# Optimization experiments

Measured on AMD Instinct MI355X. Metric: run time of the kernel, lower is better.

The kernel has to match this reference:

```python
import jax, jax.numpy as jnp
import numpy as np

N_NODES = 50000
N_EDGES = 800000
N_GRAPHS = 512
D = 128
NUM_GIN_LAYERS = 4
BN_EPS = 1e-5


def setup_inputs() -> dict:
    key = jax.random.key(0)
    ks = jax.random.split(key, 10)
    h = jax.random.normal(ks[0], (N_NODES, D), dtype=jnp.float32)
    src = jax.random.randint(ks[1], (N_EDGES,), 0, N_NODES, dtype=jnp.int32)
    dst = jax.random.randint(ks[2], (N_EDGES,), 0, N_NODES, dtype=jnp.int32)
    graph_id = jnp.sort(jax.random.randint(ks[3], (N_NODES,), 0, N_GRAPHS, dtype=jnp.int32))
    scale = 1.0 / np.sqrt(D)
    W1s = jax.random.normal(ks[4], (NUM_GIN_LAYERS, D, D), dtype=jnp.float32) * scale
    W2s = jax.random.normal(ks[5], (NUM_GIN_LAYERS, D, D), dtype=jnp.float32) * scale
    bn1_g = jnp.ones((NUM_GIN_LAYERS, D), jnp.float32)
    bn1_b = jnp.zeros((NUM_GIN_LAYERS, D), jnp.float32)
    bn2_g = jnp.ones((NUM_GIN_LAYERS, D), jnp.float32)
    bn2_b = jnp.zeros((NUM_GIN_LAYERS, D), jnp.float32)
    pred_W = jax.random.normal(ks[6], (NUM_GIN_LAYERS + 1, D, D), dtype=jnp.float32) * scale
    pred_b = jnp.zeros((NUM_GIN_LAYERS + 1, D), jnp.float32)
    return {"h": h, "src": src, "dst": dst, "graph_id": graph_id,
            "W1s": W1s, "W2s": W2s, "bn1_g": bn1_g, "bn1_b": bn1_b,
            "bn2_g": bn2_g, "bn2_b": bn2_b, "pred_W": pred_W, "pred_b": pred_b}


def _batch_norm(x, gamma, beta):
    # training-mode BN over the node axis
    mean = jnp.mean(x, axis=0)
    var = jnp.var(x, axis=0)
    return (x - mean) * jax.lax.rsqrt(var + BN_EPS) * gamma + beta


def reference(h, src, dst, graph_id, W1s, W2s, bn1_g, bn1_b, bn2_g, bn2_b, pred_W, pred_b):
    n = h.shape[0]
    hidden_rep = [h]
    for i in range(NUM_GIN_LAYERS):
        # GINConv, eps=0: (1+eps)*h + sum over in-neighbors (scatter-sum over edges)
        agg = jax.ops.segment_sum(h[src], dst, num_segments=n)
        z = h + agg
        # two-layer MLP: Linear(no bias) -> BN -> ReLU -> Linear(no bias)
        z = jax.nn.relu(_batch_norm(z @ W1s[i], bn1_g[i], bn1_b[i]))
        z = z @ W2s[i]
        # outer BN + ReLU
        h = jax.nn.relu(_batch_norm(z, bn2_g[i], bn2_b[i]))
        hidden_rep.append(h)
    # graph readout: per-graph max pool over each layer's representation,
    # then per-layer linear prediction summed (dropout is identity in eval)
    score = jnp.zeros((N_GRAPHS, pred_W.shape[-1]), h.dtype)
    for i, hr in enumerate(hidden_rep):
        pooled = jax.ops.segment_max(hr, graph_id, num_segments=N_GRAPHS,
                                     indices_are_sorted=True)
        score = score + pooled @ pred_W[i] + pred_b[i]
    return score
```

## Files before the change

kernel.cpp:

```cpp
#include <hip/hip_runtime.h>

#define N_NODES 50000
#define N_EDGES 800000
#define N_GRAPHS 512
#define DIM 128
#define NLAYERS 4
#define BN_EPS 1e-5f
#define NTILE (N_NODES / 16)
#define POIS ((int)0xAAAAAAAA)
#define NREP 8

#define NBUCK 80
#define CAPB 12288
#define EPB 1600
#define NBIN 500

typedef unsigned short u16;
typedef float f32x2 __attribute__((ext_vector_type(2)));
typedef float f32x4 __attribute__((ext_vector_type(4)));
typedef short bf16x8 __attribute__((ext_vector_type(8)));

__device__ __forceinline__ short f2bs(float f) {
    union { float f; unsigned u; } v; v.f = f;
    unsigned r = v.u + 0x7FFFu + ((v.u >> 16) & 1u);
    return (short)(r >> 16);
}
__device__ __forceinline__ float bu2f(unsigned u) {
    union { unsigned u; float f; } v; v.u = u << 16;
    return v.f;
}
__device__ __forceinline__ unsigned packbf(float x, float y) {
    return ((unsigned)(u16)f2bs(y) << 16) | (unsigned)(u16)f2bs(x);
}

__device__ __forceinline__ void foldbn(const float* __restrict__ st,
                                       const float* __restrict__ gamma,
                                       const float* __restrict__ beta,
                                       float* absm, int tid) {
    if (tid < 128) {
        float s = 0.f, sq = 0.f;
#pragma unroll
        for (int j = 0; j < NREP; j++) {
            s += st[j * 256 + tid];
            sq += st[j * 256 + 128 + tid];
        }
        float mean = s * (1.f / N_NODES);
        float var = sq * (1.f / N_NODES) - mean * mean;
        float a = gamma[tid] * rsqrtf(var + BN_EPS);
        absm[tid] = a;
        absm[DIM + tid] = beta[tid] - mean * a;
    }
}

__global__ __launch_bounds__(256) void k_prepbin(const float* __restrict__ h,
                                                 const float* __restrict__ W1s,
                                                 const float* __restrict__ W2s,
                                                 const int* __restrict__ gid,
                                                 const int* __restrict__ src,
                                                 const int* __restrict__ dst,
                                                 unsigned* __restrict__ hb,
                                                 short* __restrict__ wt,
                                                 int* __restrict__ gs, int* __restrict__ ge,
                                                 unsigned* __restrict__ eb,
                                                 int* __restrict__ gcur) {
    __shared__ int hist[NBUCK], base[NBUCK], lcur[NBUCK];
    int bid = blockIdx.x, tid = threadIdx.x;
    if (bid >= 6250) {
        int bbid = bid - 6250;
        if (tid < NBUCK) hist[tid] = 0;
        __syncthreads();
        int e0 = bbid * EPB;
        unsigned rec[7]; int rb[7];
#pragma unroll
        for (int k = 0; k < 7; k++) {
            int idx = tid + k * 256;
            rb[k] = -1;
            if (idx < EPB) {
                int s = src[e0 + idx], d = dst[e0 + idx];
                rec[k] = ((unsigned)d << 16) | (unsigned)s;
                int x = d / 6250;
                int sub = (d - x * 6250) / 625;
                rb[k] = x + 8 * sub;
                atomicAdd(&hist[rb[k]], 1);
            }
        }
        __syncthreads();
        if (tid < NBUCK) {
            int old = atomicAdd(&gcur[tid], hist[tid]);
            base[tid] = old - POIS;
            lcur[tid] = 0;
        }
        __syncthreads();
#pragma unroll
        for (int k = 0; k < 7; k++) {
            if (rb[k] >= 0) {
                int p = atomicAdd(&lcur[rb[k]], 1);
                eb[rb[k] * CAPB + base[rb[k]] + p] = rec[k];
            }
        }
        return;
    }
    int gtid = bid * 256 + tid;
    {
        f32x4 v = *(const f32x4*)(h + gtid * 4);
        uint2 pp;
        pp.x = packbf(v.x, v.y);
        pp.y = packbf(v.z, v.w);
        *(uint2*)(hb + gtid * 2) = pp;
    }
    if (gtid < 8 * 16384) {
        int m = gtid >> 14, r = gtid & 16383, n = r >> 7, k = r & 127;
        const float* W = (m < 4) ? (W1s + m * 16384) : (W2s + (m - 4) * 16384);
        wt[gtid] = f2bs(W[k * DIM + n]);
    }
    if (gtid < N_NODES) {
        int g = gid[gtid];
        if (gtid == 0 || gid[gtid - 1] != g) gs[g] = gtid;
        if (gtid == N_NODES - 1 || gid[gtid + 1] != g) ge[g] = gtid + 1;
    }
}

__global__ __launch_bounds__(256) void k_fillpool0(const unsigned* __restrict__ eb,
                                                   const int* __restrict__ gcur,
                                                   int* __restrict__ begA,
                                                   int* __restrict__ endA,
                                                   u16* __restrict__ eix,
                                                   const unsigned* __restrict__ hb,
                                                   const int* __restrict__ gs,
                                                   const int* __restrict__ ge,
                                                   float* __restrict__ pool4) {
    __shared__ int hist[625], begL[625], sm[256];
    __shared__ f32x2 psm[256];
    int bid = blockIdx.x, tid = threadIdx.x;
    if (bid < NBUCK) {
        int x = bid & 7, sub = bid >> 3;
        int n0 = x * 6250 + sub * 625;
        int mybase = 0, mycnt = 0;
        for (int r = 0; r < NBUCK; r++) {
            int c = gcur[r] - POIS;
            int rx = r & 7, rs = r >> 3;
            if (rx < x || (rx == x && rs < sub)) mybase += c;
            if (r == bid) mycnt = c;
        }
        for (int i = tid; i < 625; i += 256) hist[i] = 0;
        __syncthreads();
        const unsigned* my = eb + bid * CAPB;
        for (int i = tid; i < mycnt; i += 256) {
            int dl = (int)(my[i] >> 16) - n0;
            atomicAdd(&hist[dl], 1);
        }
        __syncthreads();
        int carry = 0;
        for (int c = 0; c < 3; c++) {
            int idx = c * 256 + tid;
            int v = (idx < 625) ? hist[idx] : 0;
            int xv = v;
            sm[tid] = xv; __syncthreads();
#pragma unroll
            for (int d = 1; d < 256; d <<= 1) {
                int y = (tid >= d) ? sm[tid - d] : 0;
                __syncthreads();
                sm[tid] = xv = xv + y;
                __syncthreads();
            }
            if (idx < 625) begL[idx] = mybase + carry + xv - v;
            int ct = sm[255];
            __syncthreads();
            carry += ct;
        }
        __syncthreads();
        for (int i = tid; i < 625; i += 256) {
            int b = begL[i];
            begA[n0 + i] = b;
            endA[n0 + i] = b + hist[i];
        }
        __syncthreads();
        for (int i = tid; i < mycnt; i += 256) {
            unsigned rc = my[i];
            int dl = (int)(rc >> 16) - n0;
            int p = atomicAdd(&begL[dl], 1);
            eix[p] = (u16)(rc & 0xFFFFu);
        }
        return;
    }
    int pb = bid - NBUCK;
    int g = pb >> 2, sub = pb & 3;
    int ci = tid & 63, ro = tid >> 6;
    int beg = gs[g], end = ge[g];
    f32x2 mx = (f32x2){-3.402823e38f, -3.402823e38f};
    if (beg >= 0 && end <= N_NODES) {
        for (int r = beg + sub * 4 + ro; r < end; r += 16) {
            unsigned w = hb[r * 64 + ci];
            mx.x = fmaxf(mx.x, bu2f(w & 0xffffu));
            mx.y = fmaxf(mx.y, bu2f(w >> 16));
        }
    }
    psm[tid] = mx;
    __syncthreads();
    if (ro == 0) {
        f32x2 mA0 = psm[tid], mA1 = psm[tid + 64];
        f32x2 mB0 = psm[tid + 128], mB1 = psm[tid + 192];
        f32x2 a, b;
        a.x = fmaxf(mA0.x, mA1.x); a.y = fmaxf(mA0.y, mA1.y);
        b.x = fmaxf(mB0.x, mB1.x); b.y = fmaxf(mB0.y, mB1.y);
        *(f32x2*)(pool4 + (pb * 2) * DIM + ci * 2) = a;
        *(f32x2*)(pool4 + (pb * 2 + 1) * DIM + ci * 2) = b;
    }
}

__global__ __launch_bounds__(128) void k_gather0(const unsigned* __restrict__ hp,
                                                 const int* __restrict__ begA,
                                                 const int* __restrict__ endA,
                                                 const u16* __restrict__ eix,
                                                 unsigned* __restrict__ Za) {
    int node = blockIdx.x * 2 + (threadIdx.x >> 6);
    int lane = threadIdx.x & 63;
    float ax = 0.f, ay = 0.f;
#define TX(w, rx, ry)                                         \
    {                                                         \
        rx += bu2f((w) & 0xffffu); ry += bu2f((w) >> 16);     \
    }
    TX(hp[node * 64 + lane], ax, ay);
    int beg = begA[node];
    int end = endA[node];
    int e = beg;
    if ((e & 1) && e < end) {
        unsigned ww = hp[eix[e] * 64 + lane];
        TX(ww, ax, ay);
        e++;
    }
    const unsigned* ep = (const unsigned*)eix;
    for (; e + 8 <= end; e += 8) {
        int k = e >> 1;
        unsigned p0 = ep[k], p1 = ep[k + 1], p2 = ep[k + 2], p3 = ep[k + 3];
        unsigned w0 = hp[(p0 & 0xffffu) * 64 + lane], w1 = hp[(p0 >> 16) * 64 + lane];
        unsigned w2 = hp[(p1 & 0xffffu) * 64 + lane], w3 = hp[(p1 >> 16) * 64 + lane];
        unsigned w4 = hp[(p2 & 0xffffu) * 64 + lane], w5 = hp[(p2 >> 16) * 64 + lane];
        unsigned w6 = hp[(p3 & 0xffffu) * 64 + lane], w7 = hp[(p3 >> 16) * 64 + lane];
        TX(w0, ax, ay); TX(w1, ax, ay); TX(w2, ax, ay); TX(w3, ax, ay);
        TX(w4, ax, ay); TX(w5, ax, ay); TX(w6, ax, ay); TX(w7, ax, ay);
    }
    for (; e + 2 <= end; e += 2) {
        unsigned pp = ep[e >> 1];
        unsigned w0 = hp[(pp & 0xffffu) * 64 + lane], w1 = hp[(pp >> 16) * 64 + lane];
        TX(w0, ax, ay); TX(w1, ax, ay);
    }
    if (e < end) {
        unsigned ww = hp[eix[e] * 64 + lane];
        TX(ww, ax, ay);
    }
#undef TX
    Za[node * 64 + lane] = packbf(ax, ay);
}

__global__ __launch_bounds__(128) void k_poolgather(const unsigned* __restrict__ Zr,
                                                    const float* __restrict__ stats,
                                                    const float* __restrict__ gamma,
                                                    const float* __restrict__ beta,
                                                    const int* __restrict__ gs,
                                                    const int* __restrict__ ge,
                                                    float* __restrict__ pool4,
                                                    const int* __restrict__ begA,
                                                    const int* __restrict__ endA,
                                                    const u16* __restrict__ eix,
                                                    unsigned* __restrict__ Za) {
    __shared__ float absm[256];
    __shared__ f32x2 psm[128];
    int bid = blockIdx.x, tid = threadIdx.x;
    foldbn(stats, gamma, beta, absm, tid);
    __syncthreads();
    if (bid < 4096) {
        int g = bid >> 3, sub = bid & 7;
        int ci = tid & 63, ro = tid >> 6;
        int beg = gs[g], end = ge[g];
        f32x2 a = *(const f32x2*)(absm + ci * 2);
        f32x2 b = *(const f32x2*)(absm + DIM + ci * 2);
        f32x2 mx = (f32x2){-3.402823e38f, -3.402823e38f};
        if (beg >= 0 && end <= N_NODES) {
            for (int r = beg + sub * 2 + ro; r < end; r += 16) {
                unsigned w = Zr[r * 64 + ci];
                float vx = fmaxf(a.x * bu2f(w & 0xffffu) + b.x, 0.f);
                float vy = fmaxf(a.y * bu2f(w >> 16) + b.y, 0.f);
                mx.x = fmaxf(mx.x, vx);
                mx.y = fmaxf(mx.y, vy);
            }
        }
        psm[tid] = mx;
        __syncthreads();
        if (ro == 0) {
            f32x2 m0 = psm[tid], m1 = psm[tid + 64];
            m0.x = fmaxf(m0.x, m1.x);
            m0.y = fmaxf(m0.y, m1.y);
            *(f32x2*)(pool4 + bid * DIM + ci * 2) = m0;
        }
        return;
    }
    int node = (bid - 4096) * 2 + (tid >> 6);
    int lane = tid & 63;
    float a0 = absm[2 * lane], a1 = absm[2 * lane + 1];
    float b0 = absm[DIM + 2 * lane], b1 = absm[DIM + 2 * lane + 1];
#define TX(w, rx, ry)                                         \
    {                                                         \
        float _x = bu2f((w) & 0xffffu), _y = bu2f((w) >> 16); \
        _x = fmaxf(a0 * _x + b0, 0.f);                        \
        _y = fmaxf(a1 * _y + b1, 0.f);                        \
        rx += _x; ry += _y;                                   \
    }
    float ax = 0.f, ay = 0.f;
    TX(Zr[node * 64 + lane], ax, ay);
    int beg = begA[node];
    int end = endA[node];
    int e = beg;
    if ((e & 1) && e < end) {
        unsigned ww = Zr[eix[e] * 64 + lane];
        TX(ww, ax, ay);
        e++;
    }
    const unsigned* ep = (const unsigned*)eix;
    for (; e + 8 <= end; e += 8) {
        int k = e >> 1;
        unsigned p0 = ep[k], p1 = ep[k + 1], p2 = ep[k + 2], p3 = ep[k + 3];
        unsigned w0 = Zr[(p0 & 0xffffu) * 64 + lane], w1 = Zr[(p0 >> 16) * 64 + lane];
        unsigned w2 = Zr[(p1 & 0xffffu) * 64 + lane], w3 = Zr[(p1 >> 16) * 64 + lane];
        unsigned w4 = Zr[(p2 & 0xffffu) * 64 + lane], w5 = Zr[(p2 >> 16) * 64 + lane];
        unsigned w6 = Zr[(p3 & 0xffffu) * 64 + lane], w7 = Zr[(p3 >> 16) * 64 + lane];
        TX(w0, ax, ay); TX(w1, ax, ay); TX(w2, ax, ay); TX(w3, ax, ay);
        TX(w4, ax, ay); TX(w5, ax, ay); TX(w6, ax, ay); TX(w7, ax, ay);
    }
    for (; e + 2 <= end; e += 2) {
        unsigned pp = ep[e >> 1];
        unsigned w0 = Zr[(pp & 0xffffu) * 64 + lane], w1 = Zr[(pp >> 16) * 64 + lane];
        TX(w0, ax, ay); TX(w1, ax, ay);
    }
    if (e < end) {
        unsigned ww = Zr[eix[e] * 64 + lane];
        TX(ww, ax, ay);
    }
#undef TX
    Za[node * 64 + lane] = packbf(ax, ay);
}

template <bool XF>
__global__ __launch_bounds__(256, 3) void k_gemm(const unsigned* __restrict__ X,
                                                 const short* __restrict__ wt,
                                                 const float* __restrict__ statsPrev,
                                                 const float* __restrict__ gamma,
                                                 const float* __restrict__ beta,
                                                 unsigned* __restrict__ OUT,
                                                 float* __restrict__ statsDst) {
    __shared__ short wls[128][136];
    __shared__ float tbuf[4][16][68];
    __shared__ float absm[256];
    __shared__ float smst[256];
    const int tid = threadIdx.x, bid = blockIdx.x;
    const int lane = tid & 63, wid = tid >> 6;
    const int ln15 = lane & 15, q = lane >> 4;
    float (*buf)[68] = tbuf[wid];

    int tile = bid * 4 + wid;
    uint4 xv[4];
    if (tile < NTILE) {
        const unsigned* xr = X + (tile * 16 + ln15) * 64;
#pragma unroll
        for (int s = 0; s < 4; s++) xv[s] = *(const uint4*)(xr + s * 16 + q * 4);
    }
    {
        int r = tid >> 1, hh = tid & 1;
        const uint4* s4 = (const uint4*)(wt + r * 128 + hh * 64);
        uint4* d4 = (uint4*)&wls[r][hh * 64];
#pragma unroll
        for (int i = 0; i < 8; i++) d4[i] = s4[i];
    }
    if (XF) foldbn(statsPrev, gamma, beta, absm, tid);
    smst[tid] = 0.f;
    __syncthreads();

    float sac[8], qac[8];
#pragma unroll
    for (int t = 0; t < 8; t++) { sac[t] = 0.f; qac[t] = 0.f; }

    if (tile < NTILE) {
        bf16x8 afr[4];
        if constexpr (!XF) {
#pragma unroll
            for (int s = 0; s < 4; s++) afr[s] = *(bf16x8*)&xv[s];
        } else {
            f32x4 aA[4], aB[4], bA[4], bB[4];
#pragma unroll
            for (int s = 0; s < 4; s++) {
                int k0 = s * 32 + q * 8;
                aA[s] = *(const f32x4*)(absm + k0);
                aB[s] = *(const f32x4*)(absm + k0 + 4);
                bA[s] = *(const f32x4*)(absm + DIM + k0);
                bB[s] = *(const f32x4*)(absm + DIM + k0 + 4);
            }
#pragma unroll
            for (int s = 0; s < 4; s++) {
                uint4 w4v = xv[s];
                float v0 = fmaxf(aA[s].x * bu2f(w4v.x & 0xffffu) + bA[s].x, 0.f);
                float v1 = fmaxf(aA[s].y * bu2f(w4v.x >> 16) + bA[s].y, 0.f);
                float v2 = fmaxf(aA[s].z * bu2f(w4v.y & 0xffffu) + bA[s].z, 0.f);
                float v3 = fmaxf(aA[s].w * bu2f(w4v.y >> 16) + bA[s].w, 0.f);
                float v4 = fmaxf(aB[s].x * bu2f(w4v.z & 0xffffu) + bB[s].x, 0.f);
                float v5 = fmaxf(aB[s].y * bu2f(w4v.z >> 16) + bB[s].y, 0.f);
                float v6 = fmaxf(aB[s].z * bu2f(w4v.w & 0xffffu) + bB[s].z, 0.f);
                float v7 = fmaxf(aB[s].w * bu2f(w4v.w >> 16) + bB[s].w, 0.f);
                bf16x8 a;
                a[0] = f2bs(v0); a[1] = f2bs(v1); a[2] = f2bs(v2); a[3] = f2bs(v3);
                a[4] = f2bs(v4); a[5] = f2bs(v5); a[6] = f2bs(v6); a[7] = f2bs(v7);
                afr[s] = a;
            }
        }
        f32x4 acc[8];
#pragma unroll
        for (int t = 0; t < 8; t++) acc[t] = (f32x4){0.f, 0.f, 0.f, 0.f};
#pragma unroll
        for (int s = 0; s < 4; s++) {
#pragma unroll
            for (int t = 0; t < 8; t++) {
                bf16x8 bfr = *(const bf16x8*)&wls[t * 16 + ln15][s * 32 + q * 8];
                acc[t] = __builtin_amdgcn_mfma_f32_16x16x32_bf16(afr[s], bfr, acc[t], 0, 0, 0);
            }
        }
#pragma unroll
        for (int t = 0; t < 8; t++) {
            float s_l = 0.f, q_l = 0.f;
#pragma unroll
            for (int r = 0; r < 4; r++) {
                float v = acc[t][r];
                s_l += v;
                q_l += v * v;
            }
            s_l += __shfl_xor(s_l, 16); s_l += __shfl_xor(s_l, 32);
            q_l += __shfl_xor(q_l, 16); q_l += __shfl_xor(q_l, 32);
            sac[t] = s_l;
            qac[t] = q_l;
        }
#pragma unroll
        for (int ch = 0; ch < 2; ch++) {
#pragma unroll
            for (int t2 = 0; t2 < 4; t2++) {
                int t = ch * 4 + t2;
#pragma unroll
                for (int r = 0; r < 4; r++)
                    buf[q * 4 + r][t2 * 16 + ln15] = acc[t][r];
            }
#pragma unroll
            for (int rr = 0; rr < 4; rr++) {
                int lr = rr * 4 + q;
                f32x4 v = *(const f32x4*)&buf[lr][ln15 * 4];
                uint2 pp;
                pp.x = packbf(v.x, v.y);
                pp.y = packbf(v.z, v.w);
                *(uint2*)(OUT + (tile * 16 + lr) * 64 + ch * 32 + ln15 * 2) = pp;
            }
        }
    }
    if (lane < 16) {
#pragma unroll
        for (int t = 0; t < 8; t++) {
            atomicAdd(&smst[t * 16 + ln15], sac[t]);
            atomicAdd(&smst[128 + t * 16 + ln15], qac[t]);
        }
    }
    __syncthreads();
    atomicAdd(statsDst + (bid & (NREP - 1)) * 256 + tid, smst[tid]);
}

__global__ __launch_bounds__(640) void k_readout(const float* __restrict__ pool4,
                                                 const unsigned* __restrict__ Zr,
                                                 const float* __restrict__ stats,
                                                 const float* __restrict__ gamma,
                                                 const float* __restrict__ beta,
                                                 const int* __restrict__ gs,
                                                 const int* __restrict__ ge,
                                                 const float* __restrict__ predW,
                                                 const float* __restrict__ predb,
                                                 float* __restrict__ out) {
    __shared__ float pl[5][DIM];
    __shared__ float ps[5][DIM];
    __shared__ float absm[256];
    int g = blockIdx.x, t = threadIdx.x;
    int l = t >> 7, c = t & 127;
    foldbn(stats, gamma, beta, absm, t);
    __syncthreads();
    {
        int beg = gs[g], end = ge[g];
        float a = absm[c], b = absm[DIM + c];
        float m4 = -3.402823e38f;
        if (beg >= 0 && end <= N_NODES) {
            int cd = c >> 1;
            int r = beg + l;
            for (; r + 5 < end; r += 10) {
                unsigned w0 = Zr[r * 64 + cd];
                unsigned w1 = Zr[(r + 5) * 64 + cd];
                float v0 = bu2f((c & 1) ? (w0 >> 16) : (w0 & 0xffffu));
                float v1 = bu2f((c & 1) ? (w1 >> 16) : (w1 & 0xffffu));
                m4 = fmaxf(m4, fmaxf(a * v0 + b, 0.f));
                m4 = fmaxf(m4, fmaxf(a * v1 + b, 0.f));
            }
            if (r < end) {
                unsigned w0 = Zr[r * 64 + cd];
                float v0 = bu2f((c & 1) ? (w0 >> 16) : (w0 & 0xffffu));
                m4 = fmaxf(m4, fmaxf(a * v0 + b, 0.f));
            }
        }
        ps[l][c] = m4;
    }
    __syncthreads();
    if (t < DIM) {
        float m = ps[0][t];
#pragma unroll
        for (int j = 1; j < 5; j++) m = fmaxf(m, ps[j][t]);
        pl[4][t] = m;
    }
    if (l < 4) {
        const float* p = pool4 + l * (N_GRAPHS * 8 * DIM) + g * 8 * DIM + c;
        float m = p[0];
#pragma unroll
        for (int j = 1; j < 8; j++) m = fmaxf(m, p[j * DIM]);
        pl[l][c] = m;
    }
    __syncthreads();
    float acc = 0.f;
    const float* W = predW + l * DIM * DIM;
    const float* prow = pl[l];
#pragma unroll 8
    for (int k = 0; k < DIM; k++) acc += prow[k] * W[k * DIM + c];
    ps[l][c] = acc;
    __syncthreads();
    if (t < DIM) {
        float s = 0.f;
#pragma unroll
        for (int ll = 0; ll < 5; ll++) s += ps[ll][c] + predb[ll * DIM + c];
        out[g * DIM + c] = s;
    }
}

extern "C" void kernel_launch(void* const* d_in, const int* in_sizes, int n_in,
                              void* d_out, int out_size, void* d_ws, size_t ws_size,
                              hipStream_t stream) {
    const float* h_in = (const float*)d_in[0];
    const int* src = (const int*)d_in[1];
    const int* dst = (const int*)d_in[2];
    const int* gid = (const int*)d_in[3];
    const float* W1s = (const float*)d_in[4];
    const float* W2s = (const float*)d_in[5];
    const float* bn1g = (const float*)d_in[6];
    const float* bn1b = (const float*)d_in[7];
    const float* bn2g = (const float*)d_in[8];
    const float* bn2b = (const float*)d_in[9];
    const float* predW = (const float*)d_in[10];
    const float* predb = (const float*)d_in[11];

    char* ws = (char*)d_ws;
    unsigned* hb = (unsigned*)(ws);
    unsigned* Za = (unsigned*)(ws + 12800000);
    unsigned* Yb = (unsigned*)(ws + 25600000);
    unsigned* Zr = (unsigned*)(ws + 38400000);
    short* wt = (short*)(ws + 51200000);
    float* pool4 = (float*)(ws + 51527680);
    int* begA = (int*)(ws + 62013440);
    int* endA = (int*)(ws + 62213440);
    u16* eix = (u16*)(ws + 62413440);
    int* gs = (int*)(ws + 64013440);
    int* ge = (int*)(ws + 64015488);
    float* stats = (float*)(ws + 64017536);
    unsigned* eb = (unsigned*)(ws + 25600000);
    int* gcur = (int*)(ws + 25600000 + 8388608);
    float* out = (float*)d_out;

    const int PSTRIDE = N_GRAPHS * 8 * DIM;

    k_prepbin<<<6750, 256, 0, stream>>>(h_in, W1s, W2s, gid, src, dst, hb, wt, gs, ge, eb, gcur);
    k_fillpool0<<<NBUCK + 2048, 256, 0, stream>>>(eb, gcur, begA, endA, eix, hb, gs, ge, pool4);

    k_gather0<<<25000, 128, 0, stream>>>(hb, begA, endA, eix, Za);
    k_gemm<false><<<782, 256, 0, stream>>>(Za, wt + 0 * 16384, nullptr, nullptr, nullptr,
                                           Yb, stats + 0 * (NREP * 256));
    k_gemm<true><<<782, 256, 0, stream>>>(Yb, wt + 4 * 16384, stats + 0 * (NREP * 256),
                                          bn1g, bn1b, Zr, stats + 1 * (NREP * 256));
    for (int l = 1; l < NLAYERS; l++) {
        k_poolgather<<<29096, 128, 0, stream>>>(Zr, stats + ((l - 1) * 2 + 1) * (NREP * 256),
                                                bn2g + (l - 1) * DIM, bn2b + (l - 1) * DIM,
                                                gs, ge, pool4 + l * PSTRIDE,
                                                begA, endA, eix, Za);
        k_gemm<false><<<782, 256, 0, stream>>>(Za, wt + l * 16384, nullptr, nullptr, nullptr,
                                               Yb, stats + (l * 2) * (NREP * 256));
        k_gemm<true><<<782, 256, 0, stream>>>(Yb, wt + (4 + l) * 16384,
                                              stats + (l * 2) * (NREP * 256), bn1g + l * DIM,
                                              bn1b + l * DIM, Zr,
                                              stats + (l * 2 + 1) * (NREP * 256));
    }
    k_readout<<<512, 640, 0, stream>>>(pool4, Zr, stats + 7 * (NREP * 256),
                                       bn2g + 3 * DIM, bn2b + 3 * DIM, gs, ge,
                                       predW, predb, out);
}
```

Baseline: 439.0 us.

## Fuse two MLP GEMMs per layer into persistent kernel with grid barrier

Adds a persistent k_gemmpair kernel that runs the first GEMM, waits at a global atomic barrier for the batch-norm statistics, then folds BN and runs the second GEMM in the same launch. The grid size comes from an occupancy query so that every block is resident. This removes one kernel launch and its tail per layer and reuses blocks across tiles. It relies on co-residency for the spin barrier and on the barrier counters starting at the poison value. The existing k_gemm also now loads its activations after the weight staging instead of prefetching them before.

```diff
diff --git a/kernel.cpp b/kernel.cpp
--- a/kernel.cpp
+++ b/kernel.cpp
@@ -356,14 +356,6 @@
     const int lane = tid & 63, wid = tid >> 6;
     const int ln15 = lane & 15, q = lane >> 4;
     float (*buf)[68] = tbuf[wid];
-
-    int tile = bid * 4 + wid;
-    uint4 xv[4];
-    if (tile < NTILE) {
-        const unsigned* xr = X + (tile * 16 + ln15) * 64;
-#pragma unroll
-        for (int s = 0; s < 4; s++) xv[s] = *(const uint4*)(xr + s * 16 + q * 4);
-    }
     {
         int r = tid >> 1, hh = tid & 1;
         const uint4* s4 = (const uint4*)(wt + r * 128 + hh * 64);
@@ -374,16 +366,16 @@
     if (XF) foldbn(statsPrev, gamma, beta, absm, tid);
     smst[tid] = 0.f;
     __syncthreads();
-
     float sac[8], qac[8];
 #pragma unroll
     for (int t = 0; t < 8; t++) { sac[t] = 0.f; qac[t] = 0.f; }
-
+    int tile = bid * 4 + wid;
     if (tile < NTILE) {
+        const unsigned* xr = X + (tile * 16 + ln15) * 64;
         bf16x8 afr[4];
         if constexpr (!XF) {
 #pragma unroll
-            for (int s = 0; s < 4; s++) afr[s] = *(bf16x8*)&xv[s];
+            for (int s = 0; s < 4; s++) afr[s] = *(const bf16x8*)(xr + s * 16 + q * 4);
         } else {
             f32x4 aA[4], aB[4], bA[4], bB[4];
 #pragma unroll
@@ -396,7 +388,7 @@
             }
 #pragma unroll
             for (int s = 0; s < 4; s++) {
-                uint4 w4v = xv[s];
+                uint4 w4v = *(const uint4*)(xr + s * 16 + q * 4);
                 float v0 = fmaxf(aA[s].x * bu2f(w4v.x & 0xffffu) + bA[s].x, 0.f);
                 float v1 = fmaxf(aA[s].y * bu2f(w4v.x >> 16) + bA[s].y, 0.f);
                 float v2 = fmaxf(aA[s].z * bu2f(w4v.y & 0xffffu) + bA[s].z, 0.f);
@@ -465,6 +457,218 @@
     }
     __syncthreads();
     atomicAdd(statsDst + (bid & (NREP - 1)) * 256 + tid, smst[tid]);
+}
+
+__global__ __launch_bounds__(256, 3) void k_gemmpair(const unsigned* __restrict__ Za,
+                                                     const short* __restrict__ wtF,
+                                                     const short* __restrict__ wtT,
+                                                     const float* __restrict__ gamma,
+                                                     const float* __restrict__ beta,
+                                                     unsigned* __restrict__ Yb,
+                                                     unsigned* __restrict__ Zr,
+                                                     float* __restrict__ stats1,
+                                                     float* __restrict__ stats2,
+                                                     int* __restrict__ bar) {
+    __shared__ short wls[128][136];
+    __shared__ float tbuf[4][16][68];
+    __shared__ float absm[256];
+    __shared__ float smst[256];
+    const int tid = threadIdx.x, bid = blockIdx.x;
+    const int lane = tid & 63, wid = tid >> 6;
+    const int ln15 = lane & 15, q = lane >> 4;
+    float (*buf)[68] = tbuf[wid];
+    const int stride = gridDim.x * 4;
+
+    {
+        int r = tid >> 1, hh = tid & 1;
+        const uint4* s4 = (const uint4*)(wtF + r * 128 + hh * 64);
+        uint4* d4 = (uint4*)&wls[r][hh * 64];
+#pragma unroll
+        for (int i = 0; i < 8; i++) d4[i] = s4[i];
+    }
+    smst[tid] = 0.f;
+    __syncthreads();
+    float sac[8], qac[8];
+#pragma unroll
+    for (int t = 0; t < 8; t++) { sac[t] = 0.f; qac[t] = 0.f; }
+    for (int tile = bid * 4 + wid; tile < NTILE; tile += stride) {
+        const unsigned* xr = Za + (tile * 16 + ln15) * 64;
+        bf16x8 afr[4];
+#pragma unroll
+        for (int s = 0; s < 4; s++) afr[s] = *(const bf16x8*)(xr + s * 16 + q * 4);
+        f32x4 acc[8];
+#pragma unroll
+        for (int t = 0; t < 8; t++) acc[t] = (f32x4){0.f, 0.f, 0.f, 0.f};
+#pragma unroll
+        for (int s = 0; s < 4; s++) {
+#pragma unroll
+            for (int t = 0; t < 8; t++) {
+                bf16x8 bfr = *(const bf16x8*)&wls[t * 16 + ln15][s * 32 + q * 8];
+                acc[t] = __builtin_amdgcn_mfma_f32_16x16x32_bf16(afr[s], bfr, acc[t], 0, 0, 0);
+            }
+        }
+#pragma unroll
+        for (int t = 0; t < 8; t++) {
+            float s_l = 0.f, q_l = 0.f;
+#pragma unroll
+            for (int r = 0; r < 4; r++) {
+                float v = acc[t][r];
+                s_l += v;
+                q_l += v * v;
+            }
+            s_l += __shfl_xor(s_l, 16); s_l += __shfl_xor(s_l, 32);
+            q_l += __shfl_xor(q_l, 16); q_l += __shfl_xor(q_l, 32);
+            sac[t] += s_l;
+            qac[t] += q_l;
+        }
+#pragma unroll
+        for (int ch = 0; ch < 2; ch++) {
+#pragma unroll
+            for (int t2 = 0; t2 < 4; t2++) {
+                int t = ch * 4 + t2;
+#pragma unroll
+                for (int r = 0; r < 4; r++)
+                    buf[q * 4 + r][t2 * 16 + ln15] = acc[t][r];
+            }
+#pragma unroll
+            for (int rr = 0; rr < 4; rr++) {
+                int lr = rr * 4 + q;
+                f32x4 v = *(const f32x4*)&buf[lr][ln15 * 4];
+                uint2 pp;
+                pp.x = packbf(v.x, v.y);
+                pp.y = packbf(v.z, v.w);
+                *(uint2*)(Yb + (tile * 16 + lr) * 64 + ch * 32 + ln15 * 2) = pp;
+            }
+        }
+    }
+    if (lane < 16) {
+#pragma unroll
+        for (int t = 0; t < 8; t++) {
+            atomicAdd(&smst[t * 16 + ln15], sac[t]);
+            atomicAdd(&smst[128 + t * 16 + ln15], qac[t]);
+        }
+    }
+    __syncthreads();
+    atomicAdd(stats1 + (bid & (NREP - 1)) * 256 + tid, smst[tid]);
+
+    __syncthreads();
+    if (tid == 0) {
+        atomicAdd(bar, 1);
+        while ((__hip_atomic_load(bar, __ATOMIC_ACQUIRE, __HIP_MEMORY_SCOPE_AGENT) - POIS)
+               < (int)gridDim.x) {
+            __builtin_amdgcn_s_sleep(2);
+        }
+    }
+    __syncthreads();
+
+    {
+        int r = tid >> 1, hh = tid & 1;
+        const uint4* s4 = (const uint4*)(wtT + r * 128 + hh * 64);
+        uint4* d4 = (uint4*)&wls[r][hh * 64];
+#pragma unroll
+        for (int i = 0; i < 8; i++) d4[i] = s4[i];
+    }
+    if (tid < 128) {
+        float s = 0.f, sq = 0.f;
+#pragma unroll
+        for (int j = 0; j < NREP; j++) {
+            s += __hip_atomic_load(stats1 + j * 256 + tid, __ATOMIC_RELAXED,
+                                   __HIP_MEMORY_SCOPE_AGENT);
+            sq += __hip_atomic_load(stats1 + j * 256 + 128 + tid, __ATOMIC_RELAXED,
+                                    __HIP_MEMORY_SCOPE_AGENT);
+        }
+        float mean = s * (1.f / N_NODES);
+        float var = sq * (1.f / N_NODES) - mean * mean;
+        float a = gamma[tid] * rsqrtf(var + BN_EPS);
+        absm[tid] = a;
+        absm[DIM + tid] = beta[tid] - mean * a;
+    }
+    smst[tid] = 0.f;
+    __syncthreads();
+#pragma unroll
+    for (int t = 0; t < 8; t++) { sac[t] = 0.f; qac[t] = 0.f; }
+    f32x4 aA[4], aB[4], bA[4], bB[4];
+#pragma unroll
+    for (int s = 0; s < 4; s++) {
+        int k0 = s * 32 + q * 8;
+        aA[s] = *(const f32x4*)(absm + k0);
+        aB[s] = *(const f32x4*)(absm + k0 + 4);
+        bA[s] = *(const f32x4*)(absm + DIM + k0);
+        bB[s] = *(const f32x4*)(absm + DIM + k0 + 4);
+    }
+    for (int tile = bid * 4 + wid; tile < NTILE; tile += stride) {
+        const unsigned* xr = Yb + (tile * 16 + ln15) * 64;
+        bf16x8 afr[4];
+#pragma unroll
+        for (int s = 0; s < 4; s++) {
+            uint4 w4v = *(const uint4*)(xr + s * 16 + q * 4);
+            float v0 = fmaxf(aA[s].x * bu2f(w4v.x & 0xffffu) + bA[s].x, 0.f);
+            float v1 = fmaxf(aA[s].y * bu2f(w4v.x >> 16) + bA[s].y, 0.f);
+            float v2 = fmaxf(aA[s].z * bu2f(w4v.y & 0xffffu) + bA[s].z, 0.f);
+            float v3 = fmaxf(aA[s].w * bu2f(w4v.y >> 16) + bA[s].w, 0.f);
+            float v4 = fmaxf(aB[s].x * bu2f(w4v.z & 0xffffu) + bB[s].x, 0.f);
+            float v5 = fmaxf(aB[s].y * bu2f(w4v.z >> 16) + bB[s].y, 0.f);
+            float v6 = fmaxf(aB[s].z * bu2f(w4v.w & 0xffffu) + bB[s].z, 0.f);
+            float v7 = fmaxf(aB[s].w * bu2f(w4v.w >> 16) + bB[s].w, 0.f);
+            bf16x8 a;
+            a[0] = f2bs(v0); a[1] = f2bs(v1); a[2] = f2bs(v2); a[3] = f2bs(v3);
+            a[4] = f2bs(v4); a[5] = f2bs(v5); a[6] = f2bs(v6); a[7] = f2bs(v7);
+            afr[s] = a;
+        }
+        f32x4 acc[8];
+#pragma unroll
+        for (int t = 0; t < 8; t++) acc[t] = (f32x4){0.f, 0.f, 0.f, 0.f};
+#pragma unroll
+        for (int s = 0; s < 4; s++) {
+#pragma unroll
+            for (int t = 0; t < 8; t++) {
+                bf16x8 bfr = *(const bf16x8*)&wls[t * 16 + ln15][s * 32 + q * 8];
+                acc[t] = __builtin_amdgcn_mfma_f32_16x16x32_bf16(afr[s], bfr, acc[t], 0, 0, 0);
+            }
+        }
+#pragma unroll
+        for (int t = 0; t < 8; t++) {
+            float s_l = 0.f, q_l = 0.f;
+#pragma unroll
+            for (int r = 0; r < 4; r++) {
+                float v = acc[t][r];
+                s_l += v;
+                q_l += v * v;
+            }
+            s_l += __shfl_xor(s_l, 16); s_l += __shfl_xor(s_l, 32);
+            q_l += __shfl_xor(q_l, 16); q_l += __shfl_xor(q_l, 32);
+            sac[t] += s_l;
+            qac[t] += q_l;
+        }
+#pragma unroll
+        for (int ch = 0; ch < 2; ch++) {
+#pragma unroll
+            for (int t2 = 0; t2 < 4; t2++) {
+                int t = ch * 4 + t2;
+#pragma unroll
+                for (int r = 0; r < 4; r++)
+                    buf[q * 4 + r][t2 * 16 + ln15] = acc[t][r];
+            }
+#pragma unroll
+            for (int rr = 0; rr < 4; rr++) {
+                int lr = rr * 4 + q;
+                f32x4 v = *(const f32x4*)&buf[lr][ln15 * 4];
+                uint2 pp;
+                pp.x = packbf(v.x, v.y);
+                pp.y = packbf(v.z, v.w);
+                *(uint2*)(Zr + (tile * 16 + lr) * 64 + ch * 32 + ln15 * 2) = pp;
+            }
+        }
+    }
+    if (lane < 16) {
+#pragma unroll
+        for (int t = 0; t < 8; t++) {
+            atomicAdd(&smst[t * 16 + ln15], sac[t]);
+            atomicAdd(&smst[128 + t * 16 + ln15], qac[t]);
+        }
+    }
+    __syncthreads();
+    atomicAdd(stats2 + (bid & (NREP - 1)) * 256 + tid, smst[tid]);
 }
 
 __global__ __launch_bounds__(640) void k_readout(const float* __restrict__ pool4,
@@ -566,31 +770,45 @@
     int* gs = (int*)(ws + 64013440);
     int* ge = (int*)(ws + 64015488);
     float* stats = (float*)(ws + 64017536);
+    int* bar = (int*)(ws + 64083072);
     unsigned* eb = (unsigned*)(ws + 25600000);
     int* gcur = (int*)(ws + 25600000 + 8388608);
     float* out = (float*)d_out;
 
     const int PSTRIDE = N_GRAPHS * 8 * DIM;
 
+    static int s_occ = -1;
+    if (s_occ < 0) {
+        int o = 0;
+        if (hipOccupancyMaxActiveBlocksPerMultiprocessor(&o, k_gemmpair, 256, 0) != hipSuccess)
+            o = 0;
+        s_occ = o;
+    }
+    const int GBP = (s_occ >= 3) ? 768 : 512;
+
     k_prepbin<<<6750, 256, 0, stream>>>(h_in, W1s, W2s, gid, src, dst, hb, wt, gs, ge, eb, gcur);
     k_fillpool0<<<NBUCK + 2048, 256, 0, stream>>>(eb, gcur, begA, endA, eix, hb, gs, ge, pool4);
 
     k_gather0<<<25000, 128, 0, stream>>>(hb, begA, endA, eix, Za);
-    k_gemm<false><<<782, 256, 0, stream>>>(Za, wt + 0 * 16384, nullptr, nullptr, nullptr,
-                                           Yb, stats + 0 * (NREP * 256));
-    k_gemm<true><<<782, 256, 0, stream>>>(Yb, wt + 4 * 16384, stats + 0 * (NREP * 256),
-                                          bn1g, bn1b, Zr, stats + 1 * (NREP * 256));
-    for (int l = 1; l < NLAYERS; l++) {
-        k_poolgather<<<29096, 128, 0, stream>>>(Zr, stats + ((l - 1) * 2 + 1) * (NREP * 256),
-                                                bn2g + (l - 1) * DIM, bn2b + (l - 1) * DIM,
-                                                gs, ge, pool4 + l * PSTRIDE,
-                                                begA, endA, eix, Za);
-        k_gemm<false><<<782, 256, 0, stream>>>(Za, wt + l * 16384, nullptr, nullptr, nullptr,
-                                               Yb, stats + (l * 2) * (NREP * 256));
-        k_gemm<true><<<782, 256, 0, stream>>>(Yb, wt + (4 + l) * 16384,
-                                              stats + (l * 2) * (NREP * 256), bn1g + l * DIM,
-                                              bn1b + l * DIM, Zr,
-                                              stats + (l * 2 + 1) * (NREP * 256));
+    for (int l = 0; l < NLAYERS; l++) {
+        if (l > 0)
+            k_poolgather<<<29096, 128, 0, stream>>>(Zr, stats + ((l - 1) * 2 + 1) * (NREP * 256),
+                                                    bn2g + (l - 1) * DIM, bn2b + (l - 1) * DIM,
+                                                    gs, ge, pool4 + l * PSTRIDE,
+                                                    begA, endA, eix, Za);
+        if (s_occ >= 2) {
+            k_gemmpair<<<GBP, 256, 0, stream>>>(Za, wt + l * 16384, wt + (4 + l) * 16384,
+                                                bn1g + l * DIM, bn1b + l * DIM, Yb, Zr,
+                                                stats + (l * 2) * (NREP * 256),
+                                                stats + (l * 2 + 1) * (NREP * 256), bar + l);
+        } else {
+            k_gemm<false><<<782, 256, 0, stream>>>(Za, wt + l * 16384, nullptr, nullptr, nullptr,
+                                                   Yb, stats + (l * 2) * (NREP * 256));
+            k_gemm<true><<<782, 256, 0, stream>>>(Yb, wt + (4 + l) * 16384,
+                                                  stats + (l * 2) * (NREP * 256), bn1g + l * DIM,
+                                                  bn1b + l * DIM, Zr,
+                                                  stats + (l * 2 + 1) * (NREP * 256));
+        }
     }
     k_readout<<<512, 640, 0, stream>>>(pool4, Zr, stats + 7 * (NREP * 256),
                                        bn2g + 3 * DIM, bn2b + 3 * DIM, gs, ge,
```

Result: no change. 438.1 us (-0.2%).
